# Kernel optimization log

Hardware: AMD Instinct MI355X
Metric: run time of the kernel (lower is better)

## Reference

```python
import jax, jax.numpy as jnp
import numpy as np

N_NODES = 100000
N_EDGES = 1600000
D_IN = 64
D_HID = 64
D_OUT = 64
DROP_P = 0.5


def _degree_norms(src, dst, n):
    ones = jnp.ones(src.shape[0], dtype=jnp.float32)
    deg_out = jax.ops.segment_sum(ones, src, num_segments=n)  # out-degree of src nodes
    deg_in = jax.ops.segment_sum(ones, dst, num_segments=n)   # in-degree of dst nodes
    norm_src = jnp.where(deg_out > 0, jax.lax.rsqrt(jnp.maximum(deg_out, 1.0)), 0.0)
    norm_dst = jnp.where(deg_in > 0, jax.lax.rsqrt(jnp.maximum(deg_in, 1.0)), 0.0)
    return norm_src, norm_dst


def _graph_conv(h, W, b, src, dst, norm_src, norm_dst, n, activation=None):
    # DGL GraphConv, norm='both': out = D_in^{-1/2} A (D_out^{-1/2} h) W + b
    h = h * norm_src[:, None]
    h = h @ W                      # small GEMM first (in >= out), math-equivalent
    msg = h[src]                   # gather  [E, d]
    agg = jax.ops.segment_sum(msg, dst, num_segments=n)  # scatter-add [N, d]
    out = agg * norm_dst[:, None] + b
    if activation is not None:
        out = activation(out)
    return out


def _dropout(h, key, p=DROP_P):
    keep = jax.random.bernoulli(key, 1.0 - p, h.shape)
    return jnp.where(keep, h / (1.0 - p), 0.0)


def setup_inputs() -> dict:
    key = jax.random.key(0)
    ks = jax.random.split(key, 6)
    x = jax.random.normal(ks[0], (N_NODES, D_IN), dtype=jnp.float32)
    W0 = jax.random.normal(ks[1], (D_IN, D_HID), dtype=jnp.float32) * 0.05
    W1 = jax.random.normal(ks[2], (D_HID, D_HID), dtype=jnp.float32) * 0.05
    W2 = jax.random.normal(ks[3], (D_HID, D_OUT), dtype=jnp.float32) * 0.05
    b0 = jnp.zeros((D_HID,), dtype=jnp.float32)
    b1 = jnp.zeros((D_HID,), dtype=jnp.float32)
    b2 = jnp.zeros((D_OUT,), dtype=jnp.float32)
    src = jax.random.randint(ks[4], (N_EDGES,), 0, N_NODES, dtype=jnp.int32)
    dst = jax.random.randint(ks[5], (N_EDGES,), 0, N_NODES, dtype=jnp.int32)
    return {"x": x, "W0": W0, "b0": b0, "W1": W1, "b1": b1, "W2": W2, "b2": b2,
            "src": src, "dst": dst}


def reference(x, W0, b0, W1, b1, W2, b2, src, dst):
    n = x.shape[0]
    norm_src, norm_dst = _degree_norms(src, dst, n)
    dk = jax.random.key(1)
    h = _graph_conv(x, W0, b0, src, dst, norm_src, norm_dst, n, jax.nn.relu)
    h = _dropout(h, jax.random.fold_in(dk, 0))
    h = _graph_conv(h, W1, b1, src, dst, norm_src, norm_dst, n, jax.nn.relu)
    h = _dropout(h, jax.random.fold_in(dk, 1))
    h = _graph_conv(h, W2, b2, src, dst, norm_src, norm_dst, n, None)
    return h
```

## Files before the change

### kernel.cpp

```cpp
#include <hip/hip_runtime.h>
#include <hip/hip_bf16.h>
#include <hip/hip_fp16.h>
#include <cstddef>


#define EB 4096
#define SUBCAP 1280
#define NB_SHIFT 9
#define NB_W 512
#define SLOT_S 48
#define WG 256

__host__ __device__ static inline unsigned rotl32(unsigned x, int r) {
  return (x << r) | (x >> (32 - r));
}

__host__ __device__ static inline void threefry2x32(unsigned k0, unsigned k1,
                                                    unsigned x0, unsigned x1,
                                                    unsigned& o0, unsigned& o1) {
  unsigned ks2 = k0 ^ k1 ^ 0x1BD11BDAu;
  x0 += k0; x1 += k1;
#define TF_ROUND(r) { x0 += x1; x1 = rotl32(x1, r); x1 ^= x0; }
  TF_ROUND(13) TF_ROUND(15) TF_ROUND(26) TF_ROUND(6)
  x0 += k1;  x1 += ks2 + 1u;
  TF_ROUND(17) TF_ROUND(29) TF_ROUND(16) TF_ROUND(24)
  x0 += ks2; x1 += k0 + 2u;
  TF_ROUND(13) TF_ROUND(15) TF_ROUND(26) TF_ROUND(6)
  x0 += k0;  x1 += k1 + 3u;
  TF_ROUND(17) TF_ROUND(29) TF_ROUND(16) TF_ROUND(24)
  x0 += k1;  x1 += ks2 + 4u;
  TF_ROUND(13) TF_ROUND(15) TF_ROUND(26) TF_ROUND(6)
  x0 += ks2; x1 += k0 + 5u;
#undef TF_ROUND
  o0 = x0; o1 = x1;
}

__device__ static inline float2 h2f(unsigned u) {
  return __half22float2(__builtin_bit_cast(__half2, u));
}
__device__ static inline unsigned f2h(float a, float b) {
  return __builtin_bit_cast(unsigned, __floats2half2_rn(a, b));
}


__global__ __launch_bounds__(1024) void bin_k(
    const int* __restrict__ src, const int* __restrict__ dst,
    unsigned* __restrict__ binbufD, unsigned* __restrict__ binbufS,
    int* __restrict__ cursD, int* __restrict__ cursS, int e) {
  __shared__ int hist_d[256], scan_d[256], curs_d[256], gpos_d[256];
  __shared__ int hist_s[256], scan_s[256], curs_s[256], gpos_s[256];
  __shared__ unsigned sorted_d[EB], sorted_s[EB];
  __shared__ unsigned char sbk_d[EB], sbk_s[EB];
  int tid = threadIdx.x, blk = blockIdx.x;
  int base = blk * EB;
  int cnt = e - base;
  if (cnt > EB) cnt = EB;
  int x = blk & 7;

  if (tid < 256) { hist_d[tid] = 0; hist_s[tid] = 0; }
  __syncthreads();
  for (int i = tid; i < cnt; i += 1024) {
    atomicAdd(&hist_d[dst[base + i] >> NB_SHIFT], 1);
    atomicAdd(&hist_s[src[base + i] >> NB_SHIFT], 1);
  }
  __syncthreads();
  int hd = 0, hs = 0;
  if (tid < 256) {
    hd = hist_d[tid]; scan_d[tid] = hd;
    hs = hist_s[tid]; scan_s[tid] = hs;
  }
  __syncthreads();
  for (int st = 1; st < 256; st <<= 1) {
    int ad = 0, as = 0;
    if (tid < 256 && tid >= st) { ad = scan_d[tid - st]; as = scan_s[tid - st]; }
    __syncthreads();
    if (tid < 256) { scan_d[tid] += ad; scan_s[tid] += as; }
    __syncthreads();
  }
  if (tid < 256) { curs_d[tid] = scan_d[tid] - hd; curs_s[tid] = scan_s[tid] - hs; }
  __syncthreads();
  for (int i = tid; i < cnt; i += 1024) {
    int s = src[base + i];
    int d = dst[base + i];
    int bd = d >> NB_SHIFT;
    int pd = atomicAdd(&curs_d[bd], 1);
    sorted_d[pd] = ((unsigned)(d & (NB_W - 1)) << 17) | (unsigned)s;
    sbk_d[pd] = (unsigned char)bd;
    int bs = s >> NB_SHIFT;
    int ps = atomicAdd(&curs_s[bs], 1);
    sorted_s[ps] = ((unsigned)(s & (NB_W - 1)) << 17) | (unsigned)d;
    sbk_s[ps] = (unsigned char)bs;
  }
  __syncthreads();
  if (tid < 256) {
    int c = hist_d[tid];
    gpos_d[tid] = (c > 0) ? atomicAdd(&cursD[x * 256 + tid], c) : 0;
    c = hist_s[tid];
    gpos_s[tid] = (c > 0) ? atomicAdd(&cursS[x * 256 + tid], c) : 0;
  }
  __syncthreads();
  for (int i = tid; i < cnt; i += 1024) {
    int b = sbk_d[i];
    int gp = gpos_d[b] + (i - (scan_d[b] - hist_d[b]));
    if (gp < SUBCAP)
      binbufD[((size_t)b * 8 + x) * SUBCAP + gp] = sorted_d[i];
    b = sbk_s[i];
    gp = gpos_s[b] + (i - (scan_s[b] - hist_s[b]));
    if (gp < SUBCAP)
      binbufS[((size_t)b * 8 + x) * SUBCAP + gp] = sorted_s[i];
  }
}


__global__ __launch_bounds__(1024) void role_k(
    const unsigned* __restrict__ binbufD, const unsigned* __restrict__ binbufS,
    const int* __restrict__ cursD, const int* __restrict__ cursS,
    int* __restrict__ slot, int* __restrict__ cnt_in,
    float* __restrict__ nsrc, const float* __restrict__ x,
    unsigned short* __restrict__ G0, int n, int nbuck) {
  __shared__ int lcur[NB_W];
  __shared__ float lns[NB_W];
  __shared__ int cx[8];
  int tid = threadIdx.x;
  int bb = blockIdx.x;
  int role = (bb < nbuck) ? 0 : 1;
  int b = role ? (bb - nbuck) : bb;

  const int* cursX = role ? cursS : cursD;
  if (tid < 8) {
    int c = cursX[tid * 256 + b];
    cx[tid] = (c > SUBCAP) ? SUBCAP : c;
  }
  for (int i = tid; i < NB_W; i += 1024) lcur[i] = 0;
  __syncthreads();

  if (role == 0) {
    for (int xx = 0; xx < 8; ++xx) {
      int c = cx[xx];
      const unsigned* sp = binbufD + ((size_t)b * 8 + xx) * SUBCAP;
      for (int i = tid; i < c; i += 1024) {
        unsigned v = sp[i];
        int dl = v >> 17;
        int s = (int)(v & 0x1FFFFu);
        int cc = atomicAdd(&lcur[dl], 1);
        if (cc < SLOT_S) slot[(size_t)((b << NB_SHIFT) + dl) * SLOT_S + cc] = s;
      }
    }
    __syncthreads();
    for (int i = tid; i < NB_W; i += 1024) {
      int v = (b << NB_SHIFT) + i;
      if (v < n) cnt_in[v] = lcur[i];
    }
  } else {
    for (int xx = 0; xx < 8; ++xx) {
      int c = cx[xx];
      const unsigned* sp = binbufS + ((size_t)b * 8 + xx) * SUBCAP;
      for (int i = tid; i < c; i += 1024) atomicAdd(&lcur[sp[i] >> 17], 1);
    }
    __syncthreads();
    int vbase = b << NB_SHIFT;
    for (int i = tid; i < NB_W; i += 1024) {
      int v = vbase + i;
      if (v < n) {
        int c = lcur[i];
        float ns = (c > 0) ? rsqrtf((float)c) : 0.f;
        lns[i] = ns;
        nsrc[v] = ns;
      }
    }
    __syncthreads();
    const float4* x4 = (const float4*)x;
    uint2* G2 = (uint2*)G0;
    for (int idx = tid; idx < NB_W * 16; idx += 1024) {
      int i = idx >> 4;
      int v = vbase + i;
      if (v < n) {
        float ns = lns[i];
        float4 r = x4[(size_t)v * 16 + (idx & 15)];
        G2[(size_t)v * 16 + (idx & 15)] =
            make_uint2(f2h(r.x * ns, r.y * ns), f2h(r.z * ns, r.w * ns));
      }
    }
  }
}

__global__ __launch_bounds__(WG) void layer_k(
    const unsigned short* __restrict__ G, const int* __restrict__ slot,
    const int* __restrict__ cnt_in, const float* __restrict__ nsrc,
    const float* __restrict__ W, const float* __restrict__ bias,
    unsigned short* __restrict__ GoutH, float* __restrict__ GoutF,
    int n, int mid, unsigned dk0, unsigned dk1) {
  __shared__ float4 Ws[1024];
  __shared__ __align__(16) float rows[4][272];
  const float4* W4 = (const float4*)W;
  for (int i = threadIdx.x; i < 1024; i += WG) Ws[i] = W4[i];

  int wave = threadIdx.x >> 6;
  int lane = threadIdx.x & 63;
  int g = lane >> 4;
  int l16 = lane & 15;
  int v = blockIdx.x * 16 + wave * 4 + g;
  bool valid = (v < n);
  int vc = valid ? v : (n - 1);

  int degt = valid ? cnt_in[vc] : 0;
  int deg = (degt > SLOT_S) ? SLOT_S : degt;
  const int* sl = slot + (size_t)vc * SLOT_S;
  const uint2* G2 = (const uint2*)G;

  float4 aA = make_float4(0.f, 0.f, 0.f, 0.f);
  float4 aB = make_float4(0.f, 0.f, 0.f, 0.f);
  float4 aC = make_float4(0.f, 0.f, 0.f, 0.f);
  float4 aD = make_float4(0.f, 0.f, 0.f, 0.f);
#define ACC(dst, m) { float2 lo = h2f((m).x), hi = h2f((m).y); \
    dst.x += lo.x; dst.y += lo.y; dst.z += hi.x; dst.w += hi.y; }
  int nq = deg >> 2;
  int i = 0;
  for (; i + 1 < nq; i += 2) {
    int4 q0 = *(const int4*)(sl + i * 4);
    int4 q1 = *(const int4*)(sl + i * 4 + 4);
    uint2 m0 = G2[(size_t)q0.x * 16 + l16];
    uint2 m1 = G2[(size_t)q0.y * 16 + l16];
    uint2 m2 = G2[(size_t)q0.z * 16 + l16];
    uint2 m3 = G2[(size_t)q0.w * 16 + l16];
    uint2 m4 = G2[(size_t)q1.x * 16 + l16];
    uint2 m5 = G2[(size_t)q1.y * 16 + l16];
    uint2 m6 = G2[(size_t)q1.z * 16 + l16];
    uint2 m7 = G2[(size_t)q1.w * 16 + l16];
    ACC(aA, m0) ACC(aB, m1) ACC(aC, m2) ACC(aD, m3)
    ACC(aA, m4) ACC(aB, m5) ACC(aC, m6) ACC(aD, m7)
  }
  if (i < nq) {
    int4 q0 = *(const int4*)(sl + i * 4);
    uint2 m0 = G2[(size_t)q0.x * 16 + l16];
    uint2 m1 = G2[(size_t)q0.y * 16 + l16];
    uint2 m2 = G2[(size_t)q0.z * 16 + l16];
    uint2 m3 = G2[(size_t)q0.w * 16 + l16];
    ACC(aA, m0) ACC(aB, m1) ACC(aC, m2) ACC(aD, m3)
  }
  int rem = deg & 3;
  if (rem) {
    int4 qq = *(const int4*)(sl + (deg & ~3));
    int s0 = qq.x;
    int s1 = (rem > 1) ? qq.y : s0;
    int s2 = (rem > 2) ? qq.z : s0;
    float w1 = (rem > 1) ? 1.f : 0.f;
    float w2 = (rem > 2) ? 1.f : 0.f;
    uint2 m0 = G2[(size_t)s0 * 16 + l16];
    uint2 m1 = G2[(size_t)s1 * 16 + l16];
    uint2 m2 = G2[(size_t)s2 * 16 + l16];
    ACC(aA, m0)
    { float2 lo = h2f(m1.x), hi = h2f(m1.y);
      aB.x = fmaf(w1, lo.x, aB.x); aB.y = fmaf(w1, lo.y, aB.y);
      aB.z = fmaf(w1, hi.x, aB.z); aB.w = fmaf(w1, hi.y, aB.w); }
    { float2 lo = h2f(m2.x), hi = h2f(m2.y);
      aC.x = fmaf(w2, lo.x, aC.x); aC.y = fmaf(w2, lo.y, aC.y);
      aC.z = fmaf(w2, hi.x, aC.z); aC.w = fmaf(w2, hi.y, aC.w); }
  }
#undef ACC
  float4 agg;
  agg.x = (aA.x + aB.x) + (aC.x + aD.x);
  agg.y = (aA.y + aB.y) + (aC.y + aD.y);
  agg.z = (aA.z + aB.z) + (aC.z + aD.z);
  agg.w = (aA.w + aB.w) + (aC.w + aD.w);

  float* rw = &rows[wave][g * 68];
  *(float4*)(rw + l16 * 4) = agg;
  __syncthreads();

  float4 acc = make_float4(0.f, 0.f, 0.f, 0.f);
#pragma unroll
  for (int k = 0; k < 64; ++k) {
    float a = rw[k];
    float4 w = Ws[k * 16 + l16];
    acc.x = fmaf(a, w.x, acc.x);
    acc.y = fmaf(a, w.y, acc.y);
    acc.z = fmaf(a, w.z, acc.z);
    acc.w = fmaf(a, w.w, acc.w);
  }

  float nd = (degt > 0) ? rsqrtf((float)degt) : 0.f;
  float4 b4 = ((const float4*)bias)[l16];
  float4 o;
  o.x = fmaf(acc.x, nd, b4.x);
  o.y = fmaf(acc.y, nd, b4.y);
  o.z = fmaf(acc.z, nd, b4.z);
  o.w = fmaf(acc.w, nd, b4.w);
  if (mid) {
    o.x = fmaxf(o.x, 0.f); o.y = fmaxf(o.y, 0.f);
    o.z = fmaxf(o.z, 0.f); o.w = fmaxf(o.w, 0.f);
    unsigned idx = (unsigned)(v * 64 + l16 * 4);
    unsigned r0a, r0b, r1a, r1b, r2a, r2b, r3a, r3b;
    threefry2x32(dk0, dk1, 0u, idx + 0u, r0a, r0b);
    threefry2x32(dk0, dk1, 0u, idx + 1u, r1a, r1b);
    threefry2x32(dk0, dk1, 0u, idx + 2u, r2a, r2b);
    threefry2x32(dk0, dk1, 0u, idx + 3u, r3a, r3b);
    float ns2 = 2.f * nsrc[vc];
    o.x = ((r0a ^ r0b) & 0x80000000u) ? 0.f : o.x * ns2;
    o.y = ((r1a ^ r1b) & 0x80000000u) ? 0.f : o.y * ns2;
    o.z = ((r2a ^ r2b) & 0x80000000u) ? 0.f : o.z * ns2;
    o.w = ((r3a ^ r3b) & 0x80000000u) ? 0.f : o.w * ns2;
    if (valid)
      ((uint2*)GoutH)[(size_t)v * 16 + l16] =
          make_uint2(f2h(o.x, o.y), f2h(o.z, o.w));
  } else {
    if (valid) ((float4*)GoutF)[(size_t)v * 16 + l16] = o;
  }
}


extern "C" void kernel_launch(void* const* d_in, const int* in_sizes, int n_in,
                              void* d_out, int out_size, void* d_ws, size_t ws_size,
                              hipStream_t stream) {
  const float* x  = (const float*)d_in[0];
  const float* W0 = (const float*)d_in[1];
  const float* b0 = (const float*)d_in[2];
  const float* W1 = (const float*)d_in[3];
  const float* b1 = (const float*)d_in[4];
  const float* W2 = (const float*)d_in[5];
  const float* b2 = (const float*)d_in[6];
  const int* src  = (const int*)d_in[7];
  const int* dst  = (const int*)d_in[8];
  float* out = (float*)d_out;

  const int n = in_sizes[0] / 64;
  const int e = in_sizes[7];
  const int nbuck = (n + NB_W - 1) / NB_W;
  const int nblk = (e + EB - 1) / EB;

  char* w = (char*)d_ws;
  size_t off = 0;
  auto alloc = [&](size_t bytes) -> void* {
    void* p = w + off;
    off += (bytes + 255) & ~(size_t)255;
    return p;
  };
  int*            cnt_in  = (int*)alloc((size_t)n * 4);
  float*          nsrc    = (float*)alloc((size_t)n * 4);
  int*            cursD   = (int*)alloc((size_t)8 * 256 * 4);
  int*            cursS   = (int*)alloc((size_t)8 * 256 * 4);
  unsigned*       binbufD = (unsigned*)alloc((size_t)nbuck * 8 * SUBCAP * 4);
  unsigned*       binbufS = (unsigned*)alloc((size_t)nbuck * 8 * SUBCAP * 4);
  int*            slot    = (int*)alloc((size_t)nbuck * NB_W * SLOT_S * 4);
  unsigned short* G0      = (unsigned short*)alloc((size_t)n * 64 * 2);
  unsigned short* G1      = (unsigned short*)alloc((size_t)n * 64 * 2);

  unsigned k0a, k0b, k1a, k1b;
  threefry2x32(0u, 1u, 0u, 0u, k0a, k0b);
  threefry2x32(0u, 1u, 0u, 1u, k1a, k1b);

  const int gL = (n + 15) / 16;

  hipMemsetAsync(cursD, 0, (size_t)8 * 256 * 4, stream);
  hipMemsetAsync(cursS, 0, (size_t)8 * 256 * 4, stream);

  bin_k<<<nblk, 1024, 0, stream>>>(src, dst, binbufD, binbufS,
                                   cursD, cursS, e);
  role_k<<<2 * nbuck, 1024, 0, stream>>>(binbufD, binbufS, cursD, cursS,
                                         slot, cnt_in, nsrc, x, G0, n, nbuck);

  layer_k<<<gL, WG, 0, stream>>>(G0, slot, cnt_in, nsrc, W0, b0, G1, nullptr,
                                 n, 1, k0a, k0b);
  layer_k<<<gL, WG, 0, stream>>>(G1, slot, cnt_in, nsrc, W1, b1, G0, nullptr,
                                 n, 1, k1a, k1b);
  layer_k<<<gL, WG, 0, stream>>>(G0, slot, cnt_in, nsrc, W2, b2, nullptr, out,
                                 n, 0, 0u, 0u);
}
```

Measured before the change: 264.5 us.

## Replace fixed-stride adjacency slots with per-bucket compact CSR and packed meta

Replaces the fixed 48-entry per-node slot array with a per-bucket compact CSR layout: role_k first counts in-degrees, prefix-scans padded offsets, then scatters source ids contiguously, packing offset and degree into one meta word. The source-side bin buffer shrinks to 16-bit local ids, cutting binning traffic. In layer_k the post-aggregation __syncthreads is replaced by a wave-local LDS wait, with a barrier moved after the W load. This lowers slot memory footprint and improves locality of index reads, at the cost of an extra counting pass and scan in role_k, and it caps degree at 255 and bucket capacity at BCAPE.

```diff
diff --git a/kernel.cpp b/kernel.cpp
--- a/kernel.cpp
+++ b/kernel.cpp
@@ -8,7 +8,7 @@
 #define SUBCAP 1280
 #define NB_SHIFT 9
 #define NB_W 512
-#define SLOT_S 48
+#define BCAPE 10240
 #define WG 256
 
 __host__ __device__ static inline unsigned rotl32(unsigned x, int r) {
@@ -45,11 +45,12 @@
 
 __global__ __launch_bounds__(1024) void bin_k(
     const int* __restrict__ src, const int* __restrict__ dst,
-    unsigned* __restrict__ binbufD, unsigned* __restrict__ binbufS,
+    unsigned* __restrict__ binbufD, unsigned short* __restrict__ binbufS,
     int* __restrict__ cursD, int* __restrict__ cursS, int e) {
   __shared__ int hist_d[256], scan_d[256], curs_d[256], gpos_d[256];
   __shared__ int hist_s[256], scan_s[256], curs_s[256], gpos_s[256];
-  __shared__ unsigned sorted_d[EB], sorted_s[EB];
+  __shared__ unsigned sorted_d[EB];
+  __shared__ unsigned short sorted_s[EB];
   __shared__ unsigned char sbk_d[EB], sbk_s[EB];
   int tid = threadIdx.x, blk = blockIdx.x;
   int base = blk * EB;
@@ -88,7 +89,7 @@
     sbk_d[pd] = (unsigned char)bd;
     int bs = s >> NB_SHIFT;
     int ps = atomicAdd(&curs_s[bs], 1);
-    sorted_s[ps] = ((unsigned)(s & (NB_W - 1)) << 17) | (unsigned)d;
+    sorted_s[ps] = (unsigned short)(s & (NB_W - 1));
     sbk_s[ps] = (unsigned char)bs;
   }
   __syncthreads();
@@ -113,12 +114,14 @@
 
 
 __global__ __launch_bounds__(1024) void role_k(
-    const unsigned* __restrict__ binbufD, const unsigned* __restrict__ binbufS,
+    const unsigned* __restrict__ binbufD,
+    const unsigned short* __restrict__ binbufS,
     const int* __restrict__ cursD, const int* __restrict__ cursS,
-    int* __restrict__ slot, int* __restrict__ cnt_in,
+    int* __restrict__ slot, unsigned* __restrict__ meta,
     float* __restrict__ nsrc, const float* __restrict__ x,
     unsigned short* __restrict__ G0, int n, int nbuck) {
   __shared__ int lcur[NB_W];
+  __shared__ int loff[NB_W];
   __shared__ float lns[NB_W];
   __shared__ int cx[8];
   int tid = threadIdx.x;
@@ -138,24 +141,50 @@
     for (int xx = 0; xx < 8; ++xx) {
       int c = cx[xx];
       const unsigned* sp = binbufD + ((size_t)b * 8 + xx) * SUBCAP;
+      for (int i = tid; i < c; i += 1024) atomicAdd(&lcur[sp[i] >> 17], 1);
+    }
+    __syncthreads();
+    int c4 = 0;
+    if (tid < NB_W) { c4 = (lcur[tid] + 3) & ~3; loff[tid] = c4; }
+    __syncthreads();
+    for (int st = 1; st < NB_W; st <<= 1) {
+      int a = 0;
+      if (tid < NB_W && tid >= st) a = loff[tid - st];
+      __syncthreads();
+      if (tid < NB_W) loff[tid] += a;
+      __syncthreads();
+    }
+    if (tid < NB_W) {
+      int off = loff[tid] - c4;
+      loff[tid] = off;
+      int v = (b << NB_SHIFT) + tid;
+      if (v < n) {
+        int dg = lcur[tid]; if (dg > 255) dg = 255;
+        unsigned of = (off < BCAPE) ? (unsigned)off : 0u;
+        meta[v] = (of << 8) | (unsigned)dg;
+      }
+    }
+    __syncthreads();
+    for (int i = tid; i < NB_W; i += 1024) lcur[i] = 0;
+    __syncthreads();
+    size_t sbase = (size_t)b * BCAPE;
+    for (int xx = 0; xx < 8; ++xx) {
+      int c = cx[xx];
+      const unsigned* sp = binbufD + ((size_t)b * 8 + xx) * SUBCAP;
       for (int i = tid; i < c; i += 1024) {
-        unsigned v = sp[i];
-        int dl = v >> 17;
-        int s = (int)(v & 0x1FFFFu);
+        unsigned vv = sp[i];
+        int dl = vv >> 17;
+        int s = (int)(vv & 0x1FFFFu);
         int cc = atomicAdd(&lcur[dl], 1);
-        if (cc < SLOT_S) slot[(size_t)((b << NB_SHIFT) + dl) * SLOT_S + cc] = s;
+        int p = loff[dl] + cc;
+        if (p < BCAPE) slot[sbase + p] = s;
       }
-    }
-    __syncthreads();
-    for (int i = tid; i < NB_W; i += 1024) {
-      int v = (b << NB_SHIFT) + i;
-      if (v < n) cnt_in[v] = lcur[i];
     }
   } else {
     for (int xx = 0; xx < 8; ++xx) {
       int c = cx[xx];
-      const unsigned* sp = binbufS + ((size_t)b * 8 + xx) * SUBCAP;
-      for (int i = tid; i < c; i += 1024) atomicAdd(&lcur[sp[i] >> 17], 1);
+      const unsigned short* sp = binbufS + ((size_t)b * 8 + xx) * SUBCAP;
+      for (int i = tid; i < c; i += 1024) atomicAdd(&lcur[sp[i]], 1);
     }
     __syncthreads();
     int vbase = b << NB_SHIFT;
@@ -186,7 +215,7 @@
 
 __global__ __launch_bounds__(WG) void layer_k(
     const unsigned short* __restrict__ G, const int* __restrict__ slot,
-    const int* __restrict__ cnt_in, const float* __restrict__ nsrc,
+    const unsigned* __restrict__ meta, const float* __restrict__ nsrc,
     const float* __restrict__ W, const float* __restrict__ bias,
     unsigned short* __restrict__ GoutH, float* __restrict__ GoutF,
     int n, int mid, unsigned dk0, unsigned dk1) {
@@ -194,6 +223,7 @@
   __shared__ __align__(16) float rows[4][272];
   const float4* W4 = (const float4*)W;
   for (int i = threadIdx.x; i < 1024; i += WG) Ws[i] = W4[i];
+  __syncthreads();
 
   int wave = threadIdx.x >> 6;
   int lane = threadIdx.x & 63;
@@ -203,9 +233,10 @@
   bool valid = (v < n);
   int vc = valid ? v : (n - 1);
 
-  int degt = valid ? cnt_in[vc] : 0;
-  int deg = (degt > SLOT_S) ? SLOT_S : degt;
-  const int* sl = slot + (size_t)vc * SLOT_S;
+  unsigned mt = meta[vc];
+  int degt = valid ? (int)(mt & 255u) : 0;
+  int deg = degt;
+  const int* sl = slot + (size_t)(vc >> NB_SHIFT) * BCAPE + (mt >> 8);
   const uint2* G2 = (const uint2*)G;
 
   float4 aA = make_float4(0.f, 0.f, 0.f, 0.f);
@@ -266,7 +297,8 @@
 
   float* rw = &rows[wave][g * 68];
   *(float4*)(rw + l16 * 4) = agg;
-  __syncthreads();
+  asm volatile("s_waitcnt lgkmcnt(0)" ::: "memory");
+  __builtin_amdgcn_sched_barrier(0);
 
   float4 acc = make_float4(0.f, 0.f, 0.f, 0.f);
 #pragma unroll
@@ -335,13 +367,13 @@
     off += (bytes + 255) & ~(size_t)255;
     return p;
   };
-  int*            cnt_in  = (int*)alloc((size_t)n * 4);
+  unsigned*       meta    = (unsigned*)alloc((size_t)n * 4);
   float*          nsrc    = (float*)alloc((size_t)n * 4);
   int*            cursD   = (int*)alloc((size_t)8 * 256 * 4);
   int*            cursS   = (int*)alloc((size_t)8 * 256 * 4);
   unsigned*       binbufD = (unsigned*)alloc((size_t)nbuck * 8 * SUBCAP * 4);
-  unsigned*       binbufS = (unsigned*)alloc((size_t)nbuck * 8 * SUBCAP * 4);
-  int*            slot    = (int*)alloc((size_t)nbuck * NB_W * SLOT_S * 4);
+  unsigned short* binbufS = (unsigned short*)alloc((size_t)nbuck * 8 * SUBCAP * 2);
+  int*            slot    = (int*)alloc((size_t)nbuck * BCAPE * 4);
   unsigned short* G0      = (unsigned short*)alloc((size_t)n * 64 * 2);
   unsigned short* G1      = (unsigned short*)alloc((size_t)n * 64 * 2);
 
@@ -357,12 +389,12 @@
   bin_k<<<nblk, 1024, 0, stream>>>(src, dst, binbufD, binbufS,
                                    cursD, cursS, e);
   role_k<<<2 * nbuck, 1024, 0, stream>>>(binbufD, binbufS, cursD, cursS,
-                                         slot, cnt_in, nsrc, x, G0, n, nbuck);
-
-  layer_k<<<gL, WG, 0, stream>>>(G0, slot, cnt_in, nsrc, W0, b0, G1, nullptr,
+                                         slot, meta, nsrc, x, G0, n, nbuck);
+
+  layer_k<<<gL, WG, 0, stream>>>(G0, slot, meta, nsrc, W0, b0, G1, nullptr,
                                  n, 1, k0a, k0b);
-  layer_k<<<gL, WG, 0, stream>>>(G1, slot, cnt_in, nsrc, W1, b1, G0, nullptr,
+  layer_k<<<gL, WG, 0, stream>>>(G1, slot, meta, nsrc, W1, b1, G0, nullptr,
                                  n, 1, k1a, k1b);
-  layer_k<<<gL, WG, 0, stream>>>(G0, slot, cnt_in, nsrc, W2, b2, nullptr, out,
+  layer_k<<<gL, WG, 0, stream>>>(G0, slot, meta, nsrc, W2, b2, nullptr, out,
                                  n, 0, 0u, 0u);
 }
```

Measured after the change: 261.9 us (median of 2 runs). Within noise of the previous version (-1.0%).
